# Optimization experiments

Hardware: AMD Instinct MI355X
Metric: run time of the kernel (lower is better)

## Reference

```python
import jax, jax.numpy as jnp
import numpy as np

B, N, Q, Z, G, P, L = 1, 6, 40000, 8, 4, 8, 4
EMBED = 128
C = EMBED // G  # 32 channels per group
IMG_H, IMG_W = 224, 480
PC_RANGE = (-50.0, -50.0, -4.0, 50.0, 50.0, 4.0)
LEVEL_HW = [(56, 120), (28, 60), (14, 30), (7, 15)]
BEV_H = BEV_W = 200
EPS = 1e-6


def _make_lidar2img():
    # 6 surround cameras, pinhole intrinsics, yaw-spaced extrinsics (nuScenes-like)
    fx = fy = 500.0
    cx, cy = IMG_W / 2.0, IMG_H / 2.0
    K = np.array([[fx, 0, cx, 0], [0, fy, cy, 0], [0, 0, 1, 0], [0, 0, 0, 1]], np.float32)
    A = np.array([[0, -1, 0], [0, 0, -1], [1, 0, 0]], np.float32)  # lidar->cam axis swap
    mats = []
    for i in range(N):
        yaw = 2.0 * np.pi * i / N
        cy_, sy_ = np.cos(yaw), np.sin(yaw)
        R_yaw = np.array([[cy_, sy_, 0], [-sy_, cy_, 0], [0, 0, 1]], np.float32)
        Rc = A @ R_yaw
        t = -Rc @ np.array([0.0, 0.0, 1.5], np.float32)
        E = np.eye(4, dtype=np.float32)
        E[:3, :3] = Rc
        E[:3, 3] = t
        mats.append(K @ E)
    return np.stack(mats)[None]  # [1, N, 4, 4]


def setup_inputs() -> dict:
    key = jax.random.key(0)
    ks = jax.random.split(key, 20)
    E = EMBED
    s = 0.02
    inp = {}
    for i, (h, w) in enumerate(LEVEL_HW):
        inp[f'feat{i}'] = jax.random.normal(ks[i], (B, N, G * C, h, w), jnp.float32)
    inp['query'] = jax.random.normal(ks[4], (B, Q, P, E), jnp.float32) * 0.02
    inp['query_pos'] = jax.random.uniform(ks[5], (B, Z, Q, 3), dtype=jnp.float32)
    inp['lidar2img'] = jnp.asarray(_make_lidar2img())
    inp['W_sw'] = jax.random.normal(ks[6], (E, G * L), jnp.float32) * s
    inp['b_sw'] = jnp.zeros((G * L,), jnp.float32)
    inp['pe_w1'] = jax.random.normal(ks[7], (3, 2 * E), jnp.float32) * 0.1
    inp['pe_b1'] = jnp.zeros((2 * E,), jnp.float32)
    inp['pe_w2'] = jax.random.normal(ks[8], (2 * E, E), jnp.float32) * s
    inp['pe_b2'] = jnp.zeros((E,), jnp.float32)
    inp['cw1'] = jax.random.normal(ks[9], (P * E, 4 * E), jnp.float32) * s
    inp['cb1'] = jnp.zeros((4 * E,), jnp.float32)
    inp['cw2'] = jax.random.normal(ks[10], (4 * E, 4 * E), jnp.float32) * s
    inp['cb2'] = jnp.zeros((4 * E,), jnp.float32)
    inp['cw3'] = jax.random.normal(ks[11], (4 * E, 4 * E), jnp.float32) * s
    inp['cb3'] = jnp.zeros((4 * E,), jnp.float32)
    inp['cw4'] = jax.random.normal(ks[12], (4 * E, E), jnp.float32) * s
    inp['cb4'] = jnp.zeros((E,), jnp.float32)
    return inp


def reference(feat0, feat1, feat2, feat3, query, query_pos, lidar2img,
              W_sw, b_sw, pe_w1, pe_b1, pe_w2, pe_b2,
              cw1, cb1, cw2, cb2, cw3, cb3, cw4, cb4):
    # --- decoder: 'b n (g c) h w -> (b g) n h w c' ---
    feats = []
    for f in (feat0, feat1, feat2, feat3):
        b, n, gc, h, w = f.shape
        f = f.reshape(b, n, G, C, h, w)
        f = jnp.transpose(f, (0, 2, 1, 4, 5, 3)).reshape(b * G, n, h, w, C)
        feats.append(f)

    qp = jnp.transpose(query_pos, (0, 2, 1, 3))  # [B,Q,Z,3]
    # PositionalEncodingMap: 2-layer MLP 3 -> 2E -> E
    pos_emb = jnp.maximum(qp @ pe_w1 + pe_b1, 0.0) @ pe_w2 + pe_b2  # [B,Q,Z,E]

    lo = jnp.asarray(PC_RANGE[:3], qp.dtype)
    hi = jnp.asarray(PC_RANGE[3:], qp.dtype)
    ref = qp * (hi - lo) + lo                                   # [B,Q,Z,3], Z==P
    ref = jnp.broadcast_to(ref[:, :, None, :, :], (B, Q, G, P, 3))

    # scale weights: 'b q p (g l)' -> softmax over levels
    sw = (query @ W_sw + b_sw).reshape(B, Q, P, G, L)
    sw = jax.nn.softmax(sw, axis=-1)
    sw = jnp.transpose(sw, (0, 1, 3, 2, 4))                     # [B,Q,G,P,L]

    # project 3D points to all cameras
    pts = jnp.concatenate([ref, jnp.ones_like(ref[..., :1])], -1)  # [B,Q,G,P,4]
    cam = jnp.einsum('bnij,bqgpj->bqgpni', lidar2img, pts)          # [B,Q,G,P,N,4]
    homo = cam[..., 2]
    uv = cam[..., :2] / jnp.maximum(homo, EPS)[..., None]
    u = uv[..., 0] / IMG_W
    v = uv[..., 1] / IMG_H
    valid = (homo > EPS) & (u > 0.0) & (u < 1.0) & (v > 0.0) & (v < 1.0)  # [B,Q,G,P,N]
    cam_idx = jnp.argmax(valid, axis=-1)                        # first valid camera
    any_valid = jnp.any(valid, axis=-1)
    take = lambda a: jnp.take_along_axis(a, cam_idx[..., None], axis=-1)[..., 0]
    u_sel, v_sel = take(u), take(v)                              # [B,Q,G,P]

    bg = jnp.arange(B)[:, None, None, None] * G + jnp.arange(G)[None, None, :, None]

    acc = jnp.zeros((B, Q, G, P, C), dtype=query.dtype)
    for l, f in enumerate(feats):  # multi-level bilinear sample + softmax fusion
        _, _, h, w, _ = f.shape
        # grid_sample align_corners=False, zero padding
        x = u_sel * w - 0.5
        y = v_sel * h - 0.5
        x0 = jnp.floor(x)
        y0 = jnp.floor(y)
        wx = (x - x0)[..., None]
        wy = (y - y0)[..., None]
        x0i = x0.astype(jnp.int32)
        y0i = y0.astype(jnp.int32)

        def corner(yi, xi):
            m = ((yi >= 0) & (yi < h) & (xi >= 0) & (xi < w))[..., None]
            vals = f[bg, cam_idx, jnp.clip(yi, 0, h - 1), jnp.clip(xi, 0, w - 1)]
            return vals * m.astype(vals.dtype)

        samp = (corner(y0i, x0i) * (1 - wx) * (1 - wy)
                + corner(y0i, x0i + 1) * wx * (1 - wy)
                + corner(y0i + 1, x0i) * (1 - wx) * wy
                + corner(y0i + 1, x0i + 1) * wx * wy)
        acc = acc + samp * sw[..., l][..., None]

    sampled = acc * any_valid[..., None].astype(acc.dtype)      # [B,Q,G,P,C]

    # 'b q g p c -> b q p (g c)'
    feat = jnp.transpose(sampled, (0, 1, 3, 2, 4)).reshape(B, Q, P, G * C)
    feat = feat + pos_emb
    feat = feat.reshape(B, Q, P * EMBED)

    # compressor: 4-layer MLP (1x1 conv == linear over channels)
    h1 = jnp.maximum(feat @ cw1 + cb1, 0.0)
    h2 = jnp.maximum(h1 @ cw2 + cb2, 0.0)
    h3 = jnp.maximum(h2 @ cw3 + cb3, 0.0)
    out = h3 @ cw4 + cb4                                         # [B,Q,E]
    return jnp.transpose(out, (0, 2, 1)).reshape(B, EMBED, BEV_H, BEV_W)
```

## Files before the change

### kernel.cpp

```cpp
#include <hip/hip_runtime.h>
#include <hip/hip_bf16.h>
#include <hip/hip_fp16.h>

using bf16 = __hip_bfloat16;
typedef __attribute__((ext_vector_type(8))) short short8;
typedef __attribute__((ext_vector_type(4))) float floatx4;

__device__ __forceinline__ float b2f(bf16 x) { return __bfloat162float(x); }
__device__ __forceinline__ bf16  f2b(float x) { return __float2bfloat16(x); }
__device__ __forceinline__ float u2f(unsigned x) { return __uint_as_float(x); }
__device__ __forceinline__ float ld(const void* p, size_t i, int f32) {
  return f32 ? ((const float*)p)[i] : b2f(((const bf16*)p)[i]);
}

__global__ void detect_kernel(const void* q, int* flag) {
  if (threadIdx.x == 0) {
    const unsigned short* u = (const unsigned short*)q;
    int f = 0;
    for (int i = 0; i < 128; i++) {
      unsigned e = (u[i] >> 7) & 0xFF;
      if (e >= 141) f = 1;
    }
    *flag = f;
  }
}

__global__ __launch_bounds__(256) void tfeat_kernel(const void* __restrict__ in,
                                                    __half* __restrict__ out, int h, int w,
                                                    const int* flag) {
  int f = *flag;
  int idx = blockIdx.x * 256 + threadIdx.x;
  int c = idx & 127;
  int rest = idx >> 7;
  int x = rest % w;
  int rest2 = rest / w;
  int y = rest2 % h;
  int n = rest2 / h;
  out[idx] = __float2half(ld(in, (size_t)((n * 128 + c) * h + y) * w + x, f));
}

__global__ __launch_bounds__(256) void tw_kernel(const void* __restrict__ in,
                                                 bf16* __restrict__ out, int K, int N,
                                                 const int* flag) {
  int f = *flag;
  int idx = blockIdx.x * 256 + threadIdx.x;
  if (idx >= K * N) return;
  int n = idx % N, k = idx / N;
  out[n * K + k] = f2b(ld(in, idx, f));
}

__global__ __launch_bounds__(256) void logit_proj_kernel(
    const void* __restrict__ query,
    const void* __restrict__ query_pos,
    const void* __restrict__ l2i,
    const bf16* __restrict__ wswT,
    const void* __restrict__ b_sw,
    float* __restrict__ swG,
    float* __restrict__ uG, float* __restrict__ vG, int* __restrict__ cvG,
    const int* flag) {
  const int f32 = *flag;
  const int t = threadIdx.x;
  const int lane = t & 63;
  const int wv = t >> 6;
  const int row0b = blockIdx.x * 256;
  const int row0w = row0b + wv * 64;
  const int quad = lane >> 4, l15 = lane & 15;
  __shared__ float l2iS[96];
  __shared__ float bswS[16];
  if (t < 72) l2iS[t] = ld(l2i, (t / 12) * 16 + (t % 12), f32);
  if (t >= 96 && t < 112) bswS[t - 96] = ld(b_sw, t - 96, f32);
  short8 bfr[4];
  #pragma unroll
  for (int ks = 0; ks < 4; ks++)
    bfr[ks] = *(const short8*)(&wswT[l15 * 128 + ks * 32 + quad * 8]);
  __syncthreads();
  floatx4 acc[4] = {};
  #pragma unroll
  for (int ks = 0; ks < 4; ks++) {
    #pragma unroll
    for (int mt = 0; mt < 4; mt++) {
      const size_t off = (size_t)(row0w + mt * 16 + l15) * 128 + ks * 32 + quad * 8;
      short8 af;
      if (f32) {
        const float* qf = (const float*)query + off;
        #pragma unroll
        for (int j = 0; j < 8; j++) af[j] = (short)__bfloat16_as_ushort(f2b(qf[j]));
      } else {
        af = *(const short8*)((const bf16*)query + off);
      }
      acc[mt] = __builtin_amdgcn_mfma_f32_16x16x32_bf16(af, bfr[ks], acc[mt], 0, 0, 0);
    }
  }
  const float bias = bswS[l15];
  #pragma unroll
  for (int mt = 0; mt < 4; mt++) {
    #pragma unroll
    for (int r = 0; r < 4; r++) {
      float x = acc[mt][r] + bias;
      float m = fmaxf(x, __shfl_xor(x, 1));
      m = fmaxf(m, __shfl_xor(m, 2));
      float e = expf(x - m);
      float s = e + __shfl_xor(e, 1);
      s += __shfl_xor(s, 2);
      const int rowG = row0w + mt * 16 + quad * 4 + r;
      swG[(size_t)rowG * 16 + l15] = e / s;
    }
  }
  const int row = row0b + t;
  int q = row >> 3, p = row & 7;
  float q0 = ld(query_pos, ((size_t)p * 40000 + q) * 3 + 0, f32);
  float q1 = ld(query_pos, ((size_t)p * 40000 + q) * 3 + 1, f32);
  float q2 = ld(query_pos, ((size_t)p * 40000 + q) * 3 + 2, f32);
  float px = q0 * 100.f - 50.f;
  float py = q1 * 100.f - 50.f;
  float pz = q2 * 8.f - 4.f;
  int cam = 0, found = 0;
  float usel = 0.f, vsel = 0.f;
  for (int n = 0; n < 6; n++) {
    const float* m = &l2iS[n * 12];
    float c0 = m[0] * px + m[1] * py + m[2] * pz + m[3];
    float c1 = m[4] * px + m[5] * py + m[6] * pz + m[7];
    float c2 = m[8] * px + m[9] * py + m[10] * pz + m[11];
    float d = fmaxf(c2, 1e-6f);
    float u = (c0 / d) / 480.f;
    float v = (c1 / d) / 224.f;
    int valid = (c2 > 1e-6f) && (u > 0.f) && (u < 1.f) && (v > 0.f) && (v < 1.f);
    if (valid && !found) { found = 1; cam = n; usel = u; vsel = v; }
  }
  uG[row] = usel; vG[row] = vsel; cvG[row] = cam | (found << 3);
}

__global__ __launch_bounds__(256) void gather_kernel(
    const float* __restrict__ swG, const float* __restrict__ uG,
    const float* __restrict__ vG, const int* __restrict__ cvG,
    const __half* __restrict__ ft, bf16* __restrict__ X) {
  const int t = threadIdx.x;
  const int lane = t & 63;
  const int row = blockIdx.x * 4 + (t >> 6);
  const int lvl = lane >> 4;
  const int l15 = lane & 15;
  float acc[8];
  #pragma unroll
  for (int k = 0; k < 8; k++) acc[k] = 0.f;
  const int cv = __builtin_amdgcn_readfirstlane(cvG[row]);
  if (cv & 8) {
    const float u = u2f(__builtin_amdgcn_readfirstlane(__float_as_uint(uG[row])));
    const float v = u2f(__builtin_amdgcn_readfirstlane(__float_as_uint(vG[row])));
    const int cam = cv & 7;
    const int h = 56 >> lvl;
    const int w = 120 >> lvl;
    const int fo4 = (lvl == 0) ? 0 : (lvl == 1) ? 645120 : (lvl == 2) ? 806400 : 846720;
    const int hw16 = h * w * 16;
    const float wl = swG[(size_t)row * 16 + (l15 >> 2) * 4 + lvl];
    float x = u * w - 0.5f, y = v * h - 0.5f;
    float x0f = floorf(x), y0f = floorf(y);
    float wx = x - x0f, wy = y - y0f;
    int x0 = (int)x0f, y0 = (int)y0f;
    int x0c = min(max(x0, 0), w - 1), x1c = min(max(x0 + 1, 0), w - 1);
    int y0c = min(max(y0, 0), h - 1), y1c = min(max(y0 + 1, 0), h - 1);
    float mx0 = (x0 >= 0 && x0 < w) ? wl : 0.f;
    float mx1 = (x0 + 1 < w) ? wl : 0.f;
    float my0 = (y0 >= 0 && y0 < h) ? 1.f : 0.f;
    float my1 = (y0 + 1 < h) ? 1.f : 0.f;
    const float c00 = (1.f - wx) * (1.f - wy) * mx0 * my0;
    const float c10 = wx * (1.f - wy) * mx1 * my0;
    const float c01 = (1.f - wx) * wy * mx0 * my1;
    const float c11 = wx * wy * mx1 * my1;
    const uint4* fb = (const uint4*)ft + fo4 + cam * hw16 + l15;
    const int o00 = (y0c * w + x0c) * 16;
    const int o10 = (y0c * w + x1c) * 16;
    const int o01 = (y1c * w + x0c) * 16;
    const int o11 = (y1c * w + x1c) * 16;
    const uint4 d00 = fb[o00];
    const uint4 d10 = fb[o10];
    const uint4 d01 = fb[o01];
    const uint4 d11 = fb[o11];
    #pragma unroll
    for (int c = 0; c < 4; c++) {
      const uint4& d = (c == 0) ? d00 : (c == 1) ? d10 : (c == 2) ? d01 : d11;
      const float cw = (c == 0) ? c00 : (c == 1) ? c10 : (c == 2) ? c01 : c11;
      const __half2* hp = reinterpret_cast<const __half2*>(&d);
      #pragma unroll
      for (int j = 0; j < 4; j++) {
        acc[2 * j]     += __low2float(hp[j]) * cw;
        acc[2 * j + 1] += __high2float(hp[j]) * cw;
      }
    }
    #pragma unroll
    for (int k = 0; k < 8; k++) {
      acc[k] += __shfl_xor(acc[k], 16);
      acc[k] += __shfl_xor(acc[k], 32);
    }
  }
  if (lane < 16) {
    uint4 o;
    unsigned p0 = (unsigned)(unsigned short)__bfloat16_as_ushort(f2b(acc[0]))
                | ((unsigned)(unsigned short)__bfloat16_as_ushort(f2b(acc[1])) << 16);
    unsigned p1 = (unsigned)(unsigned short)__bfloat16_as_ushort(f2b(acc[2]))
                | ((unsigned)(unsigned short)__bfloat16_as_ushort(f2b(acc[3])) << 16);
    unsigned p2 = (unsigned)(unsigned short)__bfloat16_as_ushort(f2b(acc[4]))
                | ((unsigned)(unsigned short)__bfloat16_as_ushort(f2b(acc[5])) << 16);
    unsigned p3 = (unsigned)(unsigned short)__bfloat16_as_ushort(f2b(acc[6]))
                | ((unsigned)(unsigned short)__bfloat16_as_ushort(f2b(acc[7])) << 16);
    o.x = p0; o.y = p1; o.z = p2; o.w = p3;
    ((uint4*)X)[(size_t)row * 16 + l15] = o;
  }
}

__global__ __launch_bounds__(256) void gemm_bt(
    const bf16* __restrict__ A, const bf16* __restrict__ Bt, const void* __restrict__ bias,
    bf16* __restrict__ Cd, float* __restrict__ Cf,
    int M, int N, int K, int relu, int trans_out, const int* flag) {
  __shared__ bf16 As[64 * 40];
  __shared__ bf16 Bs[64 * 40];
  const int f32 = *flag;
  const int t = threadIdx.x;
  const int bm = blockIdx.x * 64;
  const int bn = blockIdx.y * 64;
  const int wv = t >> 6, lane = t & 63;
  const int wm = (wv >> 1) * 32, wn = (wv & 1) * 32;
  const int quad = lane >> 4, l15 = lane & 15;
  const int srow = t >> 2, scol = (t & 3) * 8;
  floatx4 acc[2][2] = {};
  for (int k0 = 0; k0 < K; k0 += 32) {
    *(uint4*)(&As[srow * 40 + scol]) = *(const uint4*)(&A[(size_t)(bm + srow) * K + k0 + scol]);
    *(uint4*)(&Bs[srow * 40 + scol]) = *(const uint4*)(&Bt[(size_t)(bn + srow) * K + k0 + scol]);
    __syncthreads();
    short8 af[2], bfr[2];
    af[0]  = *(const short8*)(&As[(wm + l15) * 40 + quad * 8]);
    af[1]  = *(const short8*)(&As[(wm + 16 + l15) * 40 + quad * 8]);
    bfr[0] = *(const short8*)(&Bs[(wn + l15) * 40 + quad * 8]);
    bfr[1] = *(const short8*)(&Bs[(wn + 16 + l15) * 40 + quad * 8]);
    #pragma unroll
    for (int mi = 0; mi < 2; mi++)
      #pragma unroll
      for (int ni = 0; ni < 2; ni++)
        acc[mi][ni] = __builtin_amdgcn_mfma_f32_16x16x32_bf16(af[mi], bfr[ni], acc[mi][ni], 0, 0, 0);
    __syncthreads();
  }
  #pragma unroll
  for (int mi = 0; mi < 2; mi++)
    #pragma unroll
    for (int ni = 0; ni < 2; ni++) {
      int gn = bn + wn + ni * 16 + l15;
      float bv = ld(bias, gn, f32);
      #pragma unroll
      for (int r = 0; r < 4; r++) {
        int gm = bm + wm + mi * 16 + quad * 4 + r;
        float v = acc[mi][ni][r] + bv;
        if (relu) v = fmaxf(v, 0.f);
        if (trans_out) Cf[(size_t)gn * M + gm] = v;
        else           Cd[(size_t)gm * N + gn] = f2b(v);
      }
    }
}

__global__ __launch_bounds__(256) void gemm_pe(
    const void* __restrict__ query_pos, const void* __restrict__ pe_w1,
    const void* __restrict__ pe_b1, const void* __restrict__ pe_b2,
    const bf16* __restrict__ pw2t, bf16* __restrict__ X, const int* flag) {
  __shared__ bf16 As[64 * 40];
  __shared__ bf16 Bs[128 * 40];
  __shared__ float w1S[256 * 4];
  __shared__ float qpS[64 * 3];
  const int f32 = *flag;
  const int t = threadIdx.x;
  const int bm = blockIdx.x * 64;
  const int wv = t >> 6, lane = t & 63;
  const int wm = (wv & 1) * 32, wn = (wv >> 1) * 64;
  const int quad = lane >> 4, l15 = lane & 15;
  const int srow = t >> 2, scol = (t & 3) * 8;
  for (int i = t; i < 1024; i += 256) {
    int k = i >> 2, c = i & 3;
    int ku = k ^ ((k >> 3) & 7);
    w1S[ku * 4 + c] = (c < 3) ? ld(pe_w1, c * 256 + k, f32) : ld(pe_b1, k, f32);
  }
  if (t < 64) {
    int r = bm + t, qq = r >> 3, zz = r & 7;
    #pragma unroll
    for (int i = 0; i < 3; i++)
      qpS[t * 3 + i] = ld(query_pos, ((size_t)zz * 40000 + qq) * 3 + i, f32);
  }
  __syncthreads();
  const float a0 = qpS[srow * 3], a1 = qpS[srow * 3 + 1], a2 = qpS[srow * 3 + 2];
  floatx4 acc[2][4] = {};
  for (int k0 = 0; k0 < 256; k0 += 32) {
    short8 hv;
    #pragma unroll
    for (int j = 0; j < 8; j++) {
      int k = k0 + scol + j;
      int ku = k ^ ((k >> 3) & 7);
      const float* wr = &w1S[ku * 4];
      float h = fmaf(a0, wr[0], fmaf(a1, wr[1], fmaf(a2, wr[2], wr[3])));
      hv[j] = (short)__bfloat16_as_ushort(f2b(fmaxf(h, 0.f)));
    }
    *(short8*)(&As[srow * 40 + scol]) = hv;
    #pragma unroll
    for (int rep = 0; rep < 2; rep++) {
      int linear = rep * 256 + t;
      int brow = linear >> 2, bcol = (linear & 3) * 8;
      *(uint4*)(&Bs[brow * 40 + bcol]) =
          *(const uint4*)(&pw2t[(size_t)brow * 256 + k0 + bcol]);
    }
    __syncthreads();
    short8 af[2], bfr[4];
    #pragma unroll
    for (int mi = 0; mi < 2; mi++)
      af[mi] = *(const short8*)(&As[(wm + mi * 16 + l15) * 40 + quad * 8]);
    #pragma unroll
    for (int ni = 0; ni < 4; ni++)
      bfr[ni] = *(const short8*)(&Bs[(wn + ni * 16 + l15) * 40 + quad * 8]);
    #pragma unroll
    for (int mi = 0; mi < 2; mi++)
      #pragma unroll
      for (int ni = 0; ni < 4; ni++)
        acc[mi][ni] = __builtin_amdgcn_mfma_f32_16x16x32_bf16(af[mi], bfr[ni], acc[mi][ni], 0, 0, 0);
    __syncthreads();
  }
  #pragma unroll
  for (int mi = 0; mi < 2; mi++)
    #pragma unroll
    for (int ni = 0; ni < 4; ni++) {
      int gn = wn + ni * 16 + l15;
      float bv = ld(pe_b2, gn, f32);
      #pragma unroll
      for (int r = 0; r < 4; r++) {
        int gm = bm + wm + mi * 16 + quad * 4 + r;
        size_t off = (size_t)gm * 128 + gn;
        X[off] = f2b(acc[mi][ni][r] + bv + b2f(X[off]));
      }
    }
}

extern "C" void kernel_launch(void* const* d_in, const int* in_sizes, int n_in,
                              void* d_out, int out_size, void* d_ws, size_t ws_size,
                              hipStream_t stream) {
  int* flag = (int*)d_ws;
  bf16* ws = (bf16*)d_ws;
  bf16* wswT = ws + 1024;
  bf16* ft   = ws + 5760;
  bf16* wt1  = ws + 6860160;
  bf16* wt2  = ws + 7384448;
  bf16* wt3  = ws + 7646592;
  bf16* wt4  = ws + 7908736;
  bf16* pw2t = ws + 7974272;
  bf16* X    = ws + 8007040;
  bf16* Ha   = ws + 48967040;
  bf16* Hb   = X;
  float* swG = (float*)Ha;
  float* uG  = (float*)(ws + 59207040);
  float* vG  = (float*)(ws + 59847040);
  int*   cvG = (int*)(ws + 60487040);

  detect_kernel<<<1, 64, 0, stream>>>(d_in[4], flag);

  tfeat_kernel<<<20160, 256, 0, stream>>>(d_in[0], (__half*)ft, 56, 120, flag);
  tfeat_kernel<<<5040, 256, 0, stream>>>(d_in[1], (__half*)(ft + 5160960), 28, 60, flag);
  tfeat_kernel<<<1260, 256, 0, stream>>>(d_in[2], (__half*)(ft + 6451200), 14, 30, flag);
  tfeat_kernel<<<315, 256, 0, stream>>>(d_in[3], (__half*)(ft + 6773760), 7, 15, flag);
  tw_kernel<<<2048, 256, 0, stream>>>(d_in[13], wt1, 1024, 512, flag);
  tw_kernel<<<1024, 256, 0, stream>>>(d_in[15], wt2, 512, 512, flag);
  tw_kernel<<<1024, 256, 0, stream>>>(d_in[17], wt3, 512, 512, flag);
  tw_kernel<<<256, 256, 0, stream>>>(d_in[19], wt4, 512, 128, flag);
  tw_kernel<<<128, 256, 0, stream>>>(d_in[11], pw2t, 256, 128, flag);
  tw_kernel<<<8, 256, 0, stream>>>(d_in[7], wswT, 128, 16, flag);

  logit_proj_kernel<<<1250, 256, 0, stream>>>(d_in[4], d_in[5], d_in[6], wswT, d_in[8],
                                              swG, uG, vG, cvG, flag);
  gather_kernel<<<80000, 256, 0, stream>>>(swG, uG, vG, cvG, (const __half*)ft, X);
  gemm_pe<<<5000, 256, 0, stream>>>(d_in[5], d_in[9], d_in[10], d_in[12],
                                    pw2t, X, flag);

  gemm_bt<<<dim3(625, 8), 256, 0, stream>>>(X,  wt1, d_in[14], Ha, nullptr, 40000, 512, 1024, 1, 0, flag);
  gemm_bt<<<dim3(625, 8), 256, 0, stream>>>(Ha, wt2, d_in[16], Hb, nullptr, 40000, 512, 512, 1, 0, flag);
  gemm_bt<<<dim3(625, 8), 256, 0, stream>>>(Hb, wt3, d_in[18], Ha, nullptr, 40000, 512, 512, 1, 0, flag);
  gemm_bt<<<dim3(625, 2), 256, 0, stream>>>(Ha, wt4, d_in[20], nullptr, (float*)d_out, 40000, 128, 512, 0, 1, flag);
}
```

Before: 798.8 us.

## Enlarge GEMM tiles to 128x128 with direct-to-LDS loads, XOR swizzle, XCD remap

The compressor MLP GEMMs move from 64x64 to 128x128 output tiles, so each wave computes a 4x4 grid of MFMA fragments and reuses each loaded fragment more. Global-to-LDS copies now use the global_load_lds builtin instead of going through registers. An XOR swizzle replaces the LDS row padding to avoid bank conflicts, and a 1D grid is remapped so consecutive tiles land on the same XCD for L2 locality. M-boundary guards handle the partial last row tile, at the cost of more accumulator registers and fewer blocks in flight.

After: 739.0 us. 7.5% less time.

```diff
diff --git a/kernel.cpp b/kernel.cpp
--- a/kernel.cpp
+++ b/kernel.cpp
@@ -11,6 +11,11 @@
 __device__ __forceinline__ float u2f(unsigned x) { return __uint_as_float(x); }
 __device__ __forceinline__ float ld(const void* p, size_t i, int f32) {
   return f32 ? ((const float*)p)[i] : b2f(((const bf16*)p)[i]);
+}
+__device__ __forceinline__ void gload16(const bf16* g, bf16* l) {
+  __builtin_amdgcn_global_load_lds(
+      (const __attribute__((address_space(1))) unsigned int*)(g),
+      (__attribute__((address_space(3))) unsigned int*)(l), 16, 0, 0);
 }
 
 __global__ void detect_kernel(const void* q, int* flag) {
@@ -210,49 +215,77 @@
 __global__ __launch_bounds__(256) void gemm_bt(
     const bf16* __restrict__ A, const bf16* __restrict__ Bt, const void* __restrict__ bias,
     bf16* __restrict__ Cd, float* __restrict__ Cf,
-    int M, int N, int K, int relu, int trans_out, const int* flag) {
-  __shared__ bf16 As[64 * 40];
-  __shared__ bf16 Bs[64 * 40];
+    int M, int N, int K, int relu, int trans_out, int nbn, const int* flag) {
+  __shared__ bf16 As[128 * 32];
+  __shared__ bf16 Bs[128 * 32];
   const int f32 = *flag;
   const int t = threadIdx.x;
-  const int bm = blockIdx.x * 64;
-  const int bn = blockIdx.y * 64;
-  const int wv = t >> 6, lane = t & 63;
-  const int wm = (wv >> 1) * 32, wn = (wv & 1) * 32;
+  const int lane = t & 63;
+  const int wv = t >> 6;
+  const int nwg = gridDim.x;
+  const int lin = blockIdx.x;
+  const int q8 = nwg >> 3, r8 = nwg & 7;
+  const int xcd = lin & 7, idx8 = lin >> 3;
+  const int swz = ((xcd < r8) ? (xcd * (q8 + 1)) : (r8 * (q8 + 1) + (xcd - r8) * q8)) + idx8;
+  const int bm = (swz / nbn) * 128;
+  const int bn = (swz % nbn) * 128;
+  const int wm = (wv >> 1) * 64, wn = (wv & 1) * 64;
   const int quad = lane >> 4, l15 = lane & 15;
-  const int srow = t >> 2, scol = (t & 3) * 8;
-  floatx4 acc[2][2] = {};
+  const int srow = lane >> 2;
+  const int scol = ((lane & 3) * 8) ^ ((lane >= 32) ? 16 : 0);
+  const int c0 = wv * 2, c1 = wv * 2 + 1;
+  int ar0 = min(bm + c0 * 16 + srow, M - 1);
+  int ar1 = min(bm + c1 * 16 + srow, M - 1);
+  const int br0 = bn + c0 * 16 + srow;
+  const int br1 = bn + c1 * 16 + srow;
+  const bf16* pa0 = A + (size_t)ar0 * K + scol;
+  const bf16* pa1 = A + (size_t)ar1 * K + scol;
+  const bf16* pb0 = Bt + (size_t)br0 * K + scol;
+  const bf16* pb1 = Bt + (size_t)br1 * K + scol;
+  bf16* la0 = &As[c0 * 512];
+  bf16* la1 = &As[c1 * 512];
+  bf16* lb0 = &Bs[c0 * 512];
+  bf16* lb1 = &Bs[c1 * 512];
+  const int axo = quad * 8 ^ ((l15 & 8) ? 16 : 0);
+  floatx4 acc[4][4] = {};
   for (int k0 = 0; k0 < K; k0 += 32) {
-    *(uint4*)(&As[srow * 40 + scol]) = *(const uint4*)(&A[(size_t)(bm + srow) * K + k0 + scol]);
-    *(uint4*)(&Bs[srow * 40 + scol]) = *(const uint4*)(&Bt[(size_t)(bn + srow) * K + k0 + scol]);
+    gload16(pa0, la0);
+    gload16(pa1, la1);
+    gload16(pb0, lb0);
+    gload16(pb1, lb1);
+    pa0 += 32; pa1 += 32; pb0 += 32; pb1 += 32;
     __syncthreads();
-    short8 af[2], bfr[2];
-    af[0]  = *(const short8*)(&As[(wm + l15) * 40 + quad * 8]);
-    af[1]  = *(const short8*)(&As[(wm + 16 + l15) * 40 + quad * 8]);
-    bfr[0] = *(const short8*)(&Bs[(wn + l15) * 40 + quad * 8]);
-    bfr[1] = *(const short8*)(&Bs[(wn + 16 + l15) * 40 + quad * 8]);
-    #pragma unroll
-    for (int mi = 0; mi < 2; mi++)
+    short8 af[4], bfr[4];
+    #pragma unroll
+    for (int i = 0; i < 4; i++) {
+      af[i]  = *(const short8*)(&As[(wm + i * 16 + l15) * 32 + axo]);
+      bfr[i] = *(const short8*)(&Bs[(wn + i * 16 + l15) * 32 + axo]);
+    }
+    #pragma unroll
+    for (int mi = 0; mi < 4; mi++)
       #pragma unroll
-      for (int ni = 0; ni < 2; ni++)
+      for (int ni = 0; ni < 4; ni++)
         acc[mi][ni] = __builtin_amdgcn_mfma_f32_16x16x32_bf16(af[mi], bfr[ni], acc[mi][ni], 0, 0, 0);
     __syncthreads();
   }
   #pragma unroll
-  for (int mi = 0; mi < 2; mi++)
-    #pragma unroll
-    for (int ni = 0; ni < 2; ni++) {
-      int gn = bn + wn + ni * 16 + l15;
-      float bv = ld(bias, gn, f32);
+  for (int ni = 0; ni < 4; ni++) {
+    const int gn = bn + wn + ni * 16 + l15;
+    const float bv = ld(bias, gn, f32);
+    #pragma unroll
+    for (int mi = 0; mi < 4; mi++) {
       #pragma unroll
       for (int r = 0; r < 4; r++) {
-        int gm = bm + wm + mi * 16 + quad * 4 + r;
-        float v = acc[mi][ni][r] + bv;
-        if (relu) v = fmaxf(v, 0.f);
-        if (trans_out) Cf[(size_t)gn * M + gm] = v;
-        else           Cd[(size_t)gm * N + gn] = f2b(v);
+        const int gm = bm + wm + mi * 16 + quad * 4 + r;
+        if (gm < M) {
+          float v = acc[mi][ni][r] + bv;
+          if (relu) v = fmaxf(v, 0.f);
+          if (trans_out) Cf[(size_t)gn * M + gm] = v;
+          else           Cd[(size_t)gm * N + gn] = f2b(v);
+        }
       }
     }
+  }
 }
 
 __global__ __launch_bounds__(256) void gemm_pe(
@@ -371,8 +404,9 @@
   gemm_pe<<<5000, 256, 0, stream>>>(d_in[5], d_in[9], d_in[10], d_in[12],
                                     pw2t, X, flag);
 
-  gemm_bt<<<dim3(625, 8), 256, 0, stream>>>(X,  wt1, d_in[14], Ha, nullptr, 40000, 512, 1024, 1, 0, flag);
-  gemm_bt<<<dim3(625, 8), 256, 0, stream>>>(Ha, wt2, d_in[16], Hb, nullptr, 40000, 512, 512, 1, 0, flag);
-  gemm_bt<<<dim3(625, 8), 256, 0, stream>>>(Hb, wt3, d_in[18], Ha, nullptr, 40000, 512, 512, 1, 0, flag);
-  gemm_bt<<<dim3(625, 2), 256, 0, stream>>>(Ha, wt4, d_in[20], nullptr, (float*)d_out, 40000, 128, 512, 0, 1, flag);
-}
+  const int nbm = 313;
+  gemm_bt<<<nbm * 4, 256, 0, stream>>>(X,  wt1, d_in[14], Ha, nullptr, 40000, 512, 1024, 1, 0, 4, flag);
+  gemm_bt<<<nbm * 4, 256, 0, stream>>>(Ha, wt2, d_in[16], Hb, nullptr, 40000, 512, 512, 1, 0, 4, flag);
+  gemm_bt<<<nbm * 4, 256, 0, stream>>>(Hb, wt3, d_in[18], Ha, nullptr, 40000, 512, 512, 1, 0, 4, flag);
+  gemm_bt<<<nbm * 1, 256, 0, stream>>>(Ha, wt4, d_in[20], nullptr, (float*)d_out, 40000, 128, 512, 0, 1, 1, flag);
+}
```
